# Optimization experiments

Hardware: AMD Instinct MI355X
Metric: run time of the kernel (lower is better)

## Reference

```python
import jax, jax.numpy as jnp
import numpy as np
from jax import lax

K = 3  # kernel size
CO = 64  # out_channels
CI = 64  # in_channels


def setup_inputs() -> dict:
    key = jax.random.key(0)
    k1, k2, k3, k4, k5 = jax.random.split(key, 5)
    x = jax.random.normal(k1, (16, CI, 128, 128), dtype=jnp.float32)
    w1 = jax.random.normal(k2, (2 * CI, 32), dtype=jnp.float32) * 0.05
    b1 = jax.random.normal(k3, (32,), dtype=jnp.float32) * 0.05
    w2 = jax.random.normal(k4, (32, CO * CI * K * K), dtype=jnp.float32) * 0.05
    b2 = jax.random.normal(k5, (CO * CI * K * K,), dtype=jnp.float32) * 0.05
    return {"x": x, "w1": w1, "b1": b1, "w2": w2, "b2": b2}


def reference(x, w1, b1, w2, b2):
    B = x.shape[0]
    # per-sample channel statistics over spatial dims (torch.std is unbiased, ddof=1)
    mean = jnp.mean(x, axis=(2, 3))                      # [B, CI]
    std = jnp.std(x, axis=(2, 3), ddof=1)                # [B, CI]
    stats = jnp.concatenate([mean, std], axis=-1)        # [B, 2*CI]
    h = jax.nn.relu(stats @ w1 + b1)                     # [B, 32]
    kernels = (h @ w2 + b2).reshape(B, CO, CI, K, K)     # per-sample conv kernels

    def conv_one(xi, wi):
        # xi: [CI,H,W], wi: [CO,CI,K,K]; stride=1, padding=1, no bias
        return lax.conv_general_dilated(
            xi[None], wi, window_strides=(1, 1), padding=[(1, 1), (1, 1)],
            dimension_numbers=("NCHW", "OIHW", "NCHW"))[0]

    return jax.vmap(conv_one)(x, kernels)                # [B, CO, H, W]
```

## Files before the change

kernel.cpp:

```cpp
#include <hip/hip_runtime.h>
#include <hip/hip_bf16.h>


#define B_ 16
#define NPIX 16384
#define KEL 36864
#define XT_RS 8320

typedef __attribute__((ext_vector_type(4))) float f32x4;
typedef __attribute__((ext_vector_type(8))) short short8;

static __device__ __forceinline__ short bf16_of(float f) {
    __hip_bfloat16 h = __float2bfloat16(f);
    return *reinterpret_cast<short*>(&h);
}

__global__ __launch_bounds__(256) void xpose_stats(const float* __restrict__ x,
                                                   short* __restrict__ xT,
                                                   float* __restrict__ part) {
    int b = blockIdx.x, cig = blockIdx.y, pt = blockIdx.z;
    int t = threadIdx.x;
    int y = pt * 8 + (t >> 5);
    int x0 = (t & 31) * 4;

    const float* xb = x + ((size_t)(b * 64 + cig * 8)) * NPIX;
    short* xTb = xT + (size_t)b * 128 * XT_RS;

    float s[8], ss[8];
    f32x4 v[8];
    #pragma unroll
    for (int c = 0; c < 8; c++) {
        v[c] = *(const f32x4*)(xb + (size_t)c * NPIX + y * 128 + x0);
        s[c]  = v[c][0] + v[c][1] + v[c][2] + v[c][3];
        ss[c] = v[c][0]*v[c][0] + v[c][1]*v[c][1] + v[c][2]*v[c][2] + v[c][3]*v[c][3];
    }
    #pragma unroll
    for (int xi = 0; xi < 4; xi++) {
        short8 o;
        #pragma unroll
        for (int c = 0; c < 8; c++) o[c] = bf16_of(v[c][xi]);
        *(short8*)(xTb + ((size_t)(y * 130 + x0 + xi + 1)) * 64 + cig * 8) = o;
    }
    if (t < 16) {
        int y2 = pt * 8 + (t & 7);
        int col = (t & 8) ? 129 : 0;
        short8 z = {0, 0, 0, 0, 0, 0, 0, 0};
        *(short8*)(xTb + ((size_t)(y2 * 130 + col)) * 64 + cig * 8) = z;
    }

    __shared__ float red[4][16];
    int lane = t & 63, w = t >> 6;
    #pragma unroll
    for (int c = 0; c < 8; c++) {
        float a = s[c], q = ss[c];
        for (int off = 32; off; off >>= 1) { a += __shfl_down(a, off); q += __shfl_down(q, off); }
        if (lane == 0) { red[w][c * 2] = a; red[w][c * 2 + 1] = q; }
    }
    __syncthreads();
    if (t < 16)
        part[((size_t)((b * 8 + cig) * 16 + pt)) * 16 + t] =
            red[0][t] + red[1][t] + red[2][t] + red[3][t];
}

__global__ __launch_bounds__(256) void kern_gen(const float* __restrict__ part,
                                                const float* __restrict__ w1,
                                                const float* __restrict__ b1,
                                                const float* __restrict__ w2,
                                                const float* __restrict__ b2,
                                                short* __restrict__ wT) {
    int chunk = blockIdx.x, b = blockIdx.y;
    __shared__ float st[128];
    __shared__ float h[32];
    int t = threadIdx.x;
    if (t < 64) {
        int cig = t >> 3, cl = t & 7;
        const float* pb = part + ((size_t)((b * 8 + cig) * 16)) * 16 + cl * 2;
        float s = 0.f, q = 0.f;
        #pragma unroll
        for (int p = 0; p < 16; p++) { s += pb[p * 16]; q += pb[p * 16 + 1]; }
        float mean = s * (1.f / NPIX);
        float var = fmaxf((q - s * mean) * (1.f / (NPIX - 1)), 0.f);
        st[t] = mean;
        st[64 + t] = sqrtf(var);
    }
    __syncthreads();
    if (t < 32) {
        float acc = b1[t];
        for (int i = 0; i < 128; i++) acc += st[i] * w1[i * 32 + t];
        h[t] = fmaxf(acc, 0.f);
    }
    __syncthreads();

    int jbase = chunk * 2304;
    float acc[9];
    #pragma unroll
    for (int tp = 0; tp < 9; tp++) acc[tp] = b2[jbase + tp * 256 + t];
    for (int i = 0; i < 32; i++) {
        float hi = h[i];
        const float* w2r = w2 + (size_t)i * KEL + jbase + t;
        #pragma unroll
        for (int tp = 0; tp < 9; tp++) acc[tp] += hi * w2r[tp * 256];
    }
    short* wb = wT + (size_t)b * KEL;
    #pragma unroll
    for (int tp = 0; tp < 9; tp++) {
        int j = jbase + tp * 256 + t;
        int co = j / 576;
        int rem = j - co * 576;
        int ci = rem / 9;
        int tap = rem - ci * 9;
        wb[co * 576 + tap * 64 + ci] = bf16_of(acc[tp]);
    }
}

__global__ __launch_bounds__(512, 2) void conv_mfma(const short* __restrict__ xT,
                                                    const short* __restrict__ wT,
                                                    float* __restrict__ out) {
    __shared__ __align__(16) short xls[6][66][64];
    __shared__ __align__(16) short wls[64][594];

    int b = blockIdx.x, xt = blockIdx.y, ytile = blockIdx.z;
    int x0 = xt * 64, y0 = ytile * 4;
    int t = threadIdx.x;
    int l = t & 63, w = t >> 6;
    int ch = w & 1, r = w >> 1;
    int l15 = l & 15, lg = l >> 4;

    const short* xTb = xT + (size_t)b * 128 * XT_RS;
    #pragma unroll
    for (int it = 0; it < 7; it++) {
        int e = it * 512 + t;
        if (e < 3168) {
            int lr = e / 528;
            int rem = e - lr * 528;
            int xcol = rem >> 3, slot = rem & 7;
            int y = y0 - 1 + lr;
            short8 v = {0, 0, 0, 0, 0, 0, 0, 0};
            if ((unsigned)y < 128u)
                v = *(const short8*)(xTb + (size_t)y * XT_RS + (x0 + xcol) * 64 + slot * 8);
            *(short8*)&xls[lr][xcol][(slot ^ (xcol & 7)) << 3] = v;
        }
    }
    const short* wTb = wT + (size_t)b * KEL;
    #pragma unroll
    for (int it = 0; it < 9; it++) {
        int e = it * 512 + t;
        int co = e / 72;
        int rem = e - co * 72;
        int tap = rem >> 3, s = rem & 7;
        short8 v = *(const short8*)(wTb + co * 576 + tap * 64 + s * 8);
        *(short8*)&wls[co][tap * 66 + s * 8] = v;
    }
    __syncthreads();

    f32x4 acc[4][2];
    #pragma unroll
    for (int n = 0; n < 4; n++)
        #pragma unroll
        for (int g = 0; g < 2; g++) acc[n][g] = (f32x4){0.f, 0.f, 0.f, 0.f};

    #pragma unroll
    for (int kp = 0; kp < 2; kp++) {
        #pragma unroll
        for (int tap = 0; tap < 9; tap++) {
            const int dy = tap / 3, dx = tap % 3;
            short8 a0 = *(const short8*)&wls[ch * 32 + l15][tap * 66 + kp * 32 + lg * 8];
            short8 a1 = *(const short8*)&wls[ch * 32 + 16 + l15][tap * 66 + kp * 32 + lg * 8];
            #pragma unroll
            for (int n = 0; n < 4; n++) {
                int xi = n * 16 + l15 + dx;
                short8 bf = *(const short8*)&xls[r + dy][xi][((kp * 4 + lg) ^ (xi & 7)) << 3];
                acc[n][0] = __builtin_amdgcn_mfma_f32_16x16x32_bf16(a0, bf, acc[n][0], 0, 0, 0);
                acc[n][1] = __builtin_amdgcn_mfma_f32_16x16x32_bf16(a1, bf, acc[n][1], 0, 0, 0);
            }
        }
    }

    #pragma unroll
    for (int g = 0; g < 2; g++) {
        float* ob = out + ((size_t)(b * 64 + ch * 32 + g * 16 + lg * 4)) * NPIX
                        + (y0 + r) * 128 + x0 + l15;
        #pragma unroll
        for (int reg = 0; reg < 4; reg++)
            #pragma unroll
            for (int n = 0; n < 4; n++)
                ob[(size_t)reg * NPIX + n * 16] = acc[n][g][reg];
    }
}

extern "C" void kernel_launch(void* const* d_in, const int* in_sizes, int n_in,
                              void* d_out, int out_size, void* d_ws, size_t ws_size,
                              hipStream_t stream) {
    const float* x  = (const float*)d_in[0];
    const float* w1 = (const float*)d_in[1];
    const float* b1 = (const float*)d_in[2];
    const float* w2 = (const float*)d_in[3];
    const float* b2 = (const float*)d_in[4];
    float* out = (float*)d_out;

    float* part = (float*)d_ws;
    short* wT = (short*)((char*)d_ws + 131072);
    short* xT = (short*)((char*)d_ws + 131072 + 1179648);

    xpose_stats<<<dim3(B_, 8, 16), 256, 0, stream>>>(x, xT, part);
    kern_gen<<<dim3(16, B_), 256, 0, stream>>>(part, w1, b1, w2, b2, wT);
    conv_mfma<<<dim3(B_, 2, 32), 512, 0, stream>>>(xT, wT, out);
}
```

Before: 69.55 us.

## Pipeline conv row loads via global_load_lds ring buffer and batch kernel generation

The conv kernel now handles 16 output rows per block instead of 4. It keeps a 10-row ring buffer in LDS that is filled with direct global-to-LDS loads, prefetching the next rows while the current ones are computed. The weights are stored pre-swizzled in a tap-major layout so they can be DMA'd straight into LDS without padding. The kernel-generation step now computes all 16 batch samples per thread, so each w2 element is read once instead of 16 times. The trade-offs are fewer conv blocks (less parallelism), a full vmcnt(0) wait plus barrier per step, and more register pressure.

Result: faster. 64.78 us (-6.9%).

```diff
diff --git a/kernel.cpp b/kernel.cpp
--- a/kernel.cpp
+++ b/kernel.cpp
@@ -68,124 +68,174 @@
                                                 const float* __restrict__ w2,
                                                 const float* __restrict__ b2,
                                                 short* __restrict__ wT) {
-    int chunk = blockIdx.x, b = blockIdx.y;
-    __shared__ float st[128];
-    __shared__ float h[32];
+    __shared__ float st[16][128];
+    __shared__ float hT[32][16];
     int t = threadIdx.x;
-    if (t < 64) {
-        int cig = t >> 3, cl = t & 7;
-        const float* pb = part + ((size_t)((b * 8 + cig) * 16)) * 16 + cl * 2;
+
+    for (int id = t; id < 1024; id += 256) {
+        int b = id >> 6, ci = id & 63;
+        const float* pb = part + ((size_t)((b * 8 + (ci >> 3)) * 16)) * 16 + (ci & 7) * 2;
         float s = 0.f, q = 0.f;
         #pragma unroll
         for (int p = 0; p < 16; p++) { s += pb[p * 16]; q += pb[p * 16 + 1]; }
         float mean = s * (1.f / NPIX);
         float var = fmaxf((q - s * mean) * (1.f / (NPIX - 1)), 0.f);
-        st[t] = mean;
-        st[64 + t] = sqrtf(var);
-    }
-    __syncthreads();
-    if (t < 32) {
-        float acc = b1[t];
-        for (int i = 0; i < 128; i++) acc += st[i] * w1[i * 32 + t];
-        h[t] = fmaxf(acc, 0.f);
-    }
-    __syncthreads();
-
-    int jbase = chunk * 2304;
-    float acc[9];
-    #pragma unroll
-    for (int tp = 0; tp < 9; tp++) acc[tp] = b2[jbase + tp * 256 + t];
+        st[b][ci] = mean;
+        st[b][64 + ci] = sqrtf(var);
+    }
+    __syncthreads();
+    for (int id = t; id < 512; id += 256) {
+        int b = id >> 5, jj = id & 31;
+        float acc = b1[jj];
+        for (int i = 0; i < 128; i++) acc += st[b][i] * w1[i * 32 + jj];
+        hT[jj][b] = fmaxf(acc, 0.f);
+    }
+    __syncthreads();
+
+    int j = blockIdx.x * 256 + t;
+    float wv[32];
+    #pragma unroll
+    for (int i = 0; i < 32; i++) wv[i] = w2[(size_t)i * KEL + j];
+    float bv = b2[j];
+
+    float acc[16];
+    #pragma unroll
+    for (int b = 0; b < 16; b++) acc[b] = bv;
+    #pragma unroll
     for (int i = 0; i < 32; i++) {
-        float hi = h[i];
-        const float* w2r = w2 + (size_t)i * KEL + jbase + t;
-        #pragma unroll
-        for (int tp = 0; tp < 9; tp++) acc[tp] += hi * w2r[tp * 256];
-    }
-    short* wb = wT + (size_t)b * KEL;
-    #pragma unroll
-    for (int tp = 0; tp < 9; tp++) {
-        int j = jbase + tp * 256 + t;
-        int co = j / 576;
-        int rem = j - co * 576;
-        int ci = rem / 9;
-        int tap = rem - ci * 9;
-        wb[co * 576 + tap * 64 + ci] = bf16_of(acc[tp]);
-    }
+        float wvi = wv[i];
+        const f32x4* hr = (const f32x4*)&hT[i][0];
+        #pragma unroll
+        for (int q4 = 0; q4 < 4; q4++) {
+            f32x4 hq = hr[q4];
+            acc[q4 * 4 + 0] += hq[0] * wvi;
+            acc[q4 * 4 + 1] += hq[1] * wvi;
+            acc[q4 * 4 + 2] += hq[2] * wvi;
+            acc[q4 * 4 + 3] += hq[3] * wvi;
+        }
+    }
+
+    int co = j / 576;
+    int rem = j - co * 576;
+    int ci = rem / 9;
+    int tap = rem - ci * 9;
+    size_t dst = (size_t)tap * 4096 + co * 64 + ((((ci >> 3) ^ (co & 7)) << 3) | (ci & 7));
+    #pragma unroll
+    for (int b = 0; b < 16; b++)
+        wT[(size_t)b * KEL + dst] = bf16_of(acc[b]);
 }
 
 __global__ __launch_bounds__(512, 2) void conv_mfma(const short* __restrict__ xT,
                                                     const short* __restrict__ wT,
                                                     float* __restrict__ out) {
-    __shared__ __align__(16) short xls[6][66][64];
-    __shared__ __align__(16) short wls[64][594];
-
-    int b = blockIdx.x, xt = blockIdx.y, ytile = blockIdx.z;
-    int x0 = xt * 64, y0 = ytile * 4;
+    __shared__ __align__(16) short xls[10 * 528 * 8];
+    __shared__ __align__(16) short wls[9 * 512 * 8];
+
+    int b = blockIdx.x, xt = blockIdx.y, ytg = blockIdx.z;
+    int x0 = xt * 64, Y0 = ytg * 16;
     int t = threadIdx.x;
     int l = t & 63, w = t >> 6;
     int ch = w & 1, r = w >> 1;
     int l15 = l & 15, lg = l >> 4;
 
     const short* xTb = xT + (size_t)b * 128 * XT_RS;
-    #pragma unroll
-    for (int it = 0; it < 7; it++) {
-        int e = it * 512 + t;
-        if (e < 3168) {
-            int lr = e / 528;
-            int rem = e - lr * 528;
-            int xcol = rem >> 3, slot = rem & 7;
-            int y = y0 - 1 + lr;
-            short8 v = {0, 0, 0, 0, 0, 0, 0, 0};
-            if ((unsigned)y < 128u)
-                v = *(const short8*)(xTb + (size_t)y * XT_RS + (x0 + xcol) * 64 + slot * 8);
-            *(short8*)&xls[lr][xcol][(slot ^ (xcol & 7)) << 3] = v;
-        }
-    }
     const short* wTb = wT + (size_t)b * KEL;
+
+#define ZROW(sl_)                                                              \
+    {   short8 z8 = {0, 0, 0, 0, 0, 0, 0, 0};                                  \
+        for (int e = t; e < 528; e += 512)                                     \
+            *(short8*)(xls + ((sl_) * 528 + e) * 8) = z8; }
+
+#define DMAROW(sl_, y_)                                                        \
+    {   _Pragma("unroll")                                                      \
+        for (int it = 0; it < 2; it++) {                                       \
+            int e = it * 512 + t;                                              \
+            if (e < 528) {                                                     \
+                int xi = e >> 3, s = e & 7;                                    \
+                const short* src = xTb + (size_t)(y_) * XT_RS                  \
+                    + (x0 + xi) * 64 + ((s ^ (xi & 7)) << 3);                  \
+                __builtin_amdgcn_global_load_lds(                              \
+                    (const __attribute__((address_space(1))) void*)src,        \
+                    (__attribute__((address_space(3))) void*)                   \
+                        (xls + ((sl_) * 528 + it * 512 + (t & ~63)) * 8),      \
+                    16, 0, 0);                                                 \
+            }                                                                  \
+        } }
+
     #pragma unroll
     for (int it = 0; it < 9; it++) {
         int e = it * 512 + t;
-        int co = e / 72;
-        int rem = e - co * 72;
-        int tap = rem >> 3, s = rem & 7;
-        short8 v = *(const short8*)(wTb + co * 576 + tap * 64 + s * 8);
-        *(short8*)&wls[co][tap * 66 + s * 8] = v;
-    }
-    __syncthreads();
-
-    f32x4 acc[4][2];
-    #pragma unroll
-    for (int n = 0; n < 4; n++)
-        #pragma unroll
-        for (int g = 0; g < 2; g++) acc[n][g] = (f32x4){0.f, 0.f, 0.f, 0.f};
-
-    #pragma unroll
-    for (int kp = 0; kp < 2; kp++) {
-        #pragma unroll
-        for (int tap = 0; tap < 9; tap++) {
-            const int dy = tap / 3, dx = tap % 3;
-            short8 a0 = *(const short8*)&wls[ch * 32 + l15][tap * 66 + kp * 32 + lg * 8];
-            short8 a1 = *(const short8*)&wls[ch * 32 + 16 + l15][tap * 66 + kp * 32 + lg * 8];
-            #pragma unroll
-            for (int n = 0; n < 4; n++) {
-                int xi = n * 16 + l15 + dx;
-                short8 bf = *(const short8*)&xls[r + dy][xi][((kp * 4 + lg) ^ (xi & 7)) << 3];
-                acc[n][0] = __builtin_amdgcn_mfma_f32_16x16x32_bf16(a0, bf, acc[n][0], 0, 0, 0);
-                acc[n][1] = __builtin_amdgcn_mfma_f32_16x16x32_bf16(a1, bf, acc[n][1], 0, 0, 0);
+        __builtin_amdgcn_global_load_lds(
+            (const __attribute__((address_space(1))) void*)(wTb + (size_t)e * 8),
+            (__attribute__((address_space(3))) void*)(wls + (it * 512 + (t & ~63)) * 8),
+            16, 0, 0);
+    }
+    #pragma unroll
+    for (int k = 0; k < 6; k++) {
+        int y = Y0 - 1 + k;
+        if (y < 0) { ZROW(k); } else { DMAROW(k, y); }
+    }
+    asm volatile("s_waitcnt vmcnt(0)" ::: "memory");
+    __syncthreads();
+
+    int rbase = 0;
+    #pragma unroll 1
+    for (int j = 0; j < 4; j++) {
+        if (j < 3) {
+            #pragma unroll
+            for (int m = 0; m < 4; m++) {
+                int sl = rbase + 6 + m; if (sl >= 10) sl -= 10;
+                int y = Y0 + 4 * j + 5 + m;
+                if (y > 127) { ZROW(sl); } else { DMAROW(sl, y); }
             }
         }
-    }
-
-    #pragma unroll
-    for (int g = 0; g < 2; g++) {
-        float* ob = out + ((size_t)(b * 64 + ch * 32 + g * 16 + lg * 4)) * NPIX
-                        + (y0 + r) * 128 + x0 + l15;
-        #pragma unroll
-        for (int reg = 0; reg < 4; reg++)
-            #pragma unroll
-            for (int n = 0; n < 4; n++)
-                ob[(size_t)reg * NPIX + n * 16] = acc[n][g][reg];
-    }
+
+        int y0 = Y0 + 4 * j;
+        f32x4 acc[4][2];
+        #pragma unroll
+        for (int n = 0; n < 4; n++)
+            #pragma unroll
+            for (int g = 0; g < 2; g++) acc[n][g] = (f32x4){0.f, 0.f, 0.f, 0.f};
+
+        #pragma unroll
+        for (int kp = 0; kp < 2; kp++) {
+            int sig = kp * 4 + lg;
+            int pa = sig ^ (l15 & 7);
+            #pragma unroll
+            for (int tap = 0; tap < 9; tap++) {
+                const int dy = tap / 3, dx = tap % 3;
+                int sl = rbase + r + dy; if (sl >= 10) sl -= 10;
+                short8 a0 = *(const short8*)&wls[(tap * 512 + (ch * 32 + l15) * 8 + pa) * 8];
+                short8 a1 = *(const short8*)&wls[(tap * 512 + (ch * 32 + 16 + l15) * 8 + pa) * 8];
+                #pragma unroll
+                for (int n = 0; n < 4; n++) {
+                    int xi = n * 16 + l15 + dx;
+                    short8 bf = *(const short8*)&xls[(sl * 528 + xi * 8 + (sig ^ (xi & 7))) * 8];
+                    acc[n][0] = __builtin_amdgcn_mfma_f32_16x16x32_bf16(a0, bf, acc[n][0], 0, 0, 0);
+                    acc[n][1] = __builtin_amdgcn_mfma_f32_16x16x32_bf16(a1, bf, acc[n][1], 0, 0, 0);
+                }
+            }
+        }
+
+        #pragma unroll
+        for (int g = 0; g < 2; g++) {
+            float* ob = out + ((size_t)(b * 64 + ch * 32 + g * 16 + lg * 4)) * NPIX
+                            + (y0 + r) * 128 + x0 + l15;
+            #pragma unroll
+            for (int reg = 0; reg < 4; reg++)
+                #pragma unroll
+                for (int n = 0; n < 4; n++)
+                    ob[(size_t)reg * NPIX + n * 16] = acc[n][g][reg];
+        }
+
+        if (j < 3) {
+            asm volatile("s_waitcnt vmcnt(0)" ::: "memory");
+            __syncthreads();
+        }
+        rbase += 4; if (rbase >= 10) rbase -= 10;
+    }
+#undef ZROW
+#undef DMAROW
 }
 
 extern "C" void kernel_launch(void* const* d_in, const int* in_sizes, int n_in,
@@ -203,6 +253,6 @@
     short* xT = (short*)((char*)d_ws + 131072 + 1179648);
 
     xpose_stats<<<dim3(B_, 8, 16), 256, 0, stream>>>(x, xT, part);
-    kern_gen<<<dim3(16, B_), 256, 0, stream>>>(part, w1, b1, w2, b2, wT);
-    conv_mfma<<<dim3(B_, 2, 32), 512, 0, stream>>>(xT, wT, out);
-}
+    kern_gen<<<dim3(144), 256, 0, stream>>>(part, w1, b1, w2, b2, wT);
+    conv_mfma<<<dim3(B_, 2, 8), 512, 0, stream>>>(xT, wT, out);
+}
```
